# Optimization experiments

Hardware: AMD Instinct MI355X
Metric: run time of the kernel (lower is better)

The kernel has to match this reference:

```python
import jax, jax.numpy as jnp
import numpy as np

N_NODES = 100_000
N_EDGES = 3_200_000
D_IN, D_EDGE, D_HID, D_OUT = 8, 4, 32, 16
NEG_SLOPE = 0.2  # PyG GATv2Conv default


def setup_inputs() -> dict:
    key = jax.random.key(0)
    ks = jax.random.split(key, 13)
    s = 0.1
    return {
        "x": jax.random.normal(ks[0], (N_NODES, D_IN), jnp.float32),
        "edge_index": jax.random.randint(ks[1], (2, N_EDGES), 0, N_NODES, dtype=jnp.int64),
        "edge_attr": jax.random.normal(ks[2], (N_EDGES, D_EDGE), jnp.float32),
        "Wl1": jax.random.normal(ks[3], (D_IN, D_HID), jnp.float32) * s,
        "Wr1": jax.random.normal(ks[4], (D_IN, D_HID), jnp.float32) * s,
        "We1": jax.random.normal(ks[5], (D_EDGE, D_HID), jnp.float32) * s,
        "att1": jax.random.normal(ks[6], (D_HID,), jnp.float32) * s,
        "b1": jnp.zeros((D_HID,), jnp.float32),
        "Wl2": jax.random.normal(ks[7], (D_HID, D_OUT), jnp.float32) * s,
        "Wr2": jax.random.normal(ks[8], (D_HID, D_OUT), jnp.float32) * s,
        "We2": jax.random.normal(ks[9], (D_EDGE, D_OUT), jnp.float32) * s,
        "att2": jax.random.normal(ks[10], (D_OUT,), jnp.float32) * s,
        "b2": jnp.zeros((D_OUT,), jnp.float32),
    }


def _segment_softmax(score, seg, n):
    m = jax.ops.segment_max(score, seg, num_segments=n)
    e = jnp.exp(score - m[seg])
    z = jax.ops.segment_sum(e, seg, num_segments=n)
    return e / z[seg]


def _gatv2(x, src, dst, ea_raw, Wl, Wr, We, att, bias, n):
    # GATv2 (heads=1): score_ij = att . leaky_relu(Wl x_j + Wr x_i + We e_ij)
    xl = x @ Wl            # [N, d]
    xr = x @ Wr            # [N, d]
    ea = ea_raw @ We       # [E, d]
    h = jax.nn.leaky_relu(xl[src] + xr[dst] + ea, NEG_SLOPE)  # [E, d]
    score = h @ att        # [E]
    alpha = _segment_softmax(score, dst, n)
    out = jax.ops.segment_sum(alpha[:, None] * xl[src], dst, num_segments=n)
    return out + bias


def reference(x, edge_index, edge_attr, Wl1, Wr1, We1, att1, b1, Wl2, Wr2, We2, att2, b2):
    n = x.shape[0]
    src, dst = edge_index[0], edge_index[1]
    # add_self_loops=True with fill_value='mean': self-loop edge_attr = mean of
    # incoming raw edge_attr per target node (0 for isolated targets)
    ones = jnp.ones((src.shape[0],), x.dtype)
    cnt = jax.ops.segment_sum(ones, dst, num_segments=n)
    loop_attr = jax.ops.segment_sum(edge_attr, dst, num_segments=n) / jnp.maximum(cnt, 1.0)[:, None]
    ar = jnp.arange(n, dtype=src.dtype)
    src2 = jnp.concatenate([src, ar])
    dst2 = jnp.concatenate([dst, ar])
    ea2 = jnp.concatenate([edge_attr, loop_attr], axis=0)
    h = jax.nn.relu(_gatv2(x, src2, dst2, ea2, Wl1, Wr1, We1, att1, b1, n))
    out = _gatv2(h, src2, dst2, ea2, Wl2, Wr2, We2, att2, b2, n)
    return out.reshape(-1)
```

## Files before the change

### kernel.cpp

```cpp
#include <hip/hip_runtime.h>

#define NEG_SLOPE 0.2f
#define CHUNK 16384
#define KMAX  1600
#define CAP   3264
#define NBLKMAX 256
#define NDB   49

__global__ __launch_bounds__(1024) void k_bin(const int* __restrict__ ei,
                                              const float* __restrict__ eattr,
                                              int* __restrict__ cloff,
                                              int* __restrict__ ssrc,
                                              float4* __restrict__ seat,
                                              int E, int K) {
    __shared__ int s_off[KMAX + 1];
    __shared__ unsigned s_eid[CHUNK];
    int t = threadIdx.x;
    for (int i = t; i <= K; i += 1024) s_off[i] = 0;
    __syncthreads();
    int base = blockIdx.x * CHUNK;
    int end = min(base + CHUNK, E);
    int Ec = end - base;
    unsigned pack[CHUNK / 1024];
#pragma unroll
    for (int i = 0; i < CHUNK / 1024; i++) {
        int el = t + 1024 * i;
        pack[i] = 0xFFFFFFFFu;
        if (el < Ec) {
            int dst = ei[E + base + el];
            int b = dst >> 6;
            int r = atomicAdd(&s_off[b], 1);
            pack[i] = ((unsigned)b << 20) | ((unsigned)(dst & 63) << 14) | (unsigned)r;
        }
    }
    __syncthreads();
    if (t < 64) {
        int run = 0;
        for (int bb = 0; bb < K; bb += 64) {
            int b = bb + t;
            int v = (b < K) ? s_off[b] : 0;
            int x = v;
#pragma unroll
            for (int off = 1; off < 64; off <<= 1) {
                int y = __shfl_up(x, off, 64);
                if (t >= off) x += y;
            }
            if (b < K) s_off[b] = run + x - v;
            run += __shfl(x, 63, 64);
        }
        if (t == 0) s_off[K] = run;
    }
    __syncthreads();
#pragma unroll
    for (int i = 0; i < CHUNK / 1024; i++) {
        int el = t + 1024 * i;
        if (el < Ec) {
            unsigned p = pack[i];
            int b = p >> 20;
            int r = p & 0x3FFF;
            int dl = (p >> 14) & 63;
            s_eid[s_off[b] + r] = ((unsigned)dl << 14) | (unsigned)el;
        }
    }
    __syncthreads();
    for (int pos = t; pos < Ec; pos += 1024) {
        unsigned v = s_eid[pos];
        int el = v & 0x3FFF;
        int dl = v >> 14;
        int e = base + el;
        int src = ei[e];
        float4 a = *(const float4*)(eattr + 4ll * e);
        ssrc[base + pos] = src | (dl << 17);
        seat[base + pos] = a;
    }
    for (int i = t; i <= K; i += 1024)
        cloff[(long long)blockIdx.x * (K + 1) + i] = s_off[i];
}

__global__ void k_transp(const int* __restrict__ in, int* __restrict__ out, int R, int C) {
    __shared__ int tile[32][33];
    int c0 = blockIdx.x * 32, r0 = blockIdx.y * 32;
    int c = c0 + threadIdx.x, r = r0 + threadIdx.y;
    if (r < R && c < C) tile[threadIdx.y][threadIdx.x] = in[(long long)r * C + c];
    __syncthreads();
    int oc = r0 + threadIdx.x, orr = c0 + threadIdx.y;
    if (orr < C && oc < R) out[(long long)orr * R + oc] = tile[threadIdx.x][threadIdx.y];
}

__global__ void k_btot(const int* __restrict__ cloffT, int* __restrict__ bucketTotal,
                       int K, int NBLK) {
    int b = (blockIdx.x * blockDim.x + threadIdx.x) >> 6;
    int lane = threadIdx.x & 63;
    if (b >= K) return;
    const int* r0 = cloffT + (long long)b * NBLK;
    const int* r1 = r0 + NBLK;
    int s = 0;
    for (int c = lane; c < NBLK; c += 64) s += r1[c] - r0[c];
#pragma unroll
    for (int off = 32; off >= 1; off >>= 1) s += __shfl_xor(s, off, 64);
    if (lane == 0) bucketTotal[b] = s;
}

__global__ void k_scanK(const int* __restrict__ bucketTotal, int* __restrict__ slotBase,
                        int* __restrict__ qofs, int N, int K) {
    __shared__ int s[512];
    int t = threadIdx.x;
    int v[4];
    int sum = 0;
    int base = t * 4;
    for (int j = 0; j < 4; j++) {
        int b = base + j, x = 0;
        if (b < K) { int nb = min(64, N - (b << 6)); x = bucketTotal[b] + nb; }
        v[j] = sum;
        sum += x;
    }
    s[t] = sum;
    __syncthreads();
    for (int off = 1; off < 512; off <<= 1) {
        int x = (t >= off) ? s[t - off] : 0;
        __syncthreads();
        s[t] += x;
        __syncthreads();
    }
    int tb = s[t] - sum;
    for (int j = 0; j < 4; j++) {
        int b = base + j;
        if (b < K) slotBase[b] = tb + v[j];
    }
    if (t == 511) { slotBase[K] = s[511]; qofs[4ll * N] = s[511]; }
}

__global__ __launch_bounds__(512, 8) void k_perm(const int* __restrict__ ssrc,
                                                 const float4* __restrict__ seat,
                                                 const int* __restrict__ cloffT,
                                                 const int* __restrict__ slotBase,
                                                 int* __restrict__ qofs,
                                                 int* __restrict__ fsrc,
                                                 float4* __restrict__ feat,
                                                 int N, int K, int NBLK, int QDIV) {
    __shared__ int s_pack[CAP];
    __shared__ int s_g[CAP];
    __shared__ int co[NBLKMAX], qq[NBLKMAX + 1], sc[NBLKMAX];
    __shared__ int hist2[256], cur2[256], lst2[256], sc2[256];
    __shared__ int hist[64];
    __shared__ float lsum[64][4];
    int b = blockIdx.x, t = threadIdx.x;
    int nb = min(64, N - (b << 6));
    if (t < 256) { hist2[t] = 0; cur2[t] = 0; }
    if (t < 64) {
        lsum[t][0] = 0.f; lsum[t][1] = 0.f; lsum[t][2] = 0.f; lsum[t][3] = 0.f;
    }
    const int* r0 = cloffT + (long long)b * NBLK;
    const int* r1 = r0 + NBLK;
    int len = 0;
    if (t < NBLKMAX) {
        if (t < NBLK) { int c0v = r0[t]; len = r1[t] - c0v; co[t] = c0v; }
        sc[t] = (t < NBLK) ? len : 0;
    }
    __syncthreads();
    for (int off = 1; off < NBLKMAX; off <<= 1) {
        int x = 0;
        if (t < NBLKMAX && t >= off) x = sc[t - off];
        __syncthreads();
        if (t < NBLKMAX) sc[t] += x;
        __syncthreads();
    }
    if (t < NBLK) qq[t] = sc[t] - len;
    if (t == NBLKMAX - 1) qq[NBLK] = sc[NBLKMAX - 1];
    __syncthreads();
    int Eb = qq[NBLK];
    for (int i = t; i < Eb; i += 512) {
        int lo2 = 0, hi2 = NBLK;
        while (lo2 + 1 < hi2) { int mid = (lo2 + hi2) >> 1; if (qq[mid] <= i) lo2 = mid; else hi2 = mid; }
        int g = lo2 * CHUNK + co[lo2] + (i - qq[lo2]);
        int p = ssrc[g];
        int srcv = p & 0x1FFFF;
        int q = (unsigned)srcv / (unsigned)QDIV;
        s_pack[i] = p | (q << 23);
        s_g[i] = g;
        atomicAdd(&hist2[(((p >> 17) & 63) << 2) | q], 1);
    }
    __syncthreads();
    if (t < 64) {
        int c = hist2[4 * t] + hist2[4 * t + 1] + hist2[4 * t + 2] + hist2[4 * t + 3];
        hist[t] = c;
        if (t < nb) {
            int node = (b << 6) + t;
            int qs = (unsigned)node / (unsigned)QDIV;
            hist2[t * 4 + qs] += 1;
            cur2[t * 4 + qs] = 1;
        }
    }
    __syncthreads();
    if (t < 256) sc2[t] = hist2[t];
    __syncthreads();
    for (int off = 1; off < 256; off <<= 1) {
        int x = 0;
        if (t < 256 && t >= off) x = sc2[t - off];
        __syncthreads();
        if (t < 256) sc2[t] += x;
        __syncthreads();
    }
    if (t < 256) lst2[t] = sc2[t] - hist2[t];
    __syncthreads();
    int lo = slotBase[b];
    if (t < 256) {
        int dl = t >> 2;
        if (dl < nb)
            qofs[(((long long)((b << 6) + dl)) << 2) + (t & 3)] = lo + lst2[t];
    }
    for (int i = t; i < Eb; i += 512) {
        int p = s_pack[i];
        int dl = (p >> 17) & 63;
        int q = (p >> 23) & 3;
        int srcv = p & 0x1FFFF;
        int bin = (dl << 2) | q;
        int r = atomicAdd(&cur2[bin], 1);
        float4 a = seat[s_g[i]];
        long long pos = lo + lst2[bin] + r;
        fsrc[pos] = srcv;
        feat[pos] = a;
        atomicAdd(&lsum[dl][0], a.x);
        atomicAdd(&lsum[dl][1], a.y);
        atomicAdd(&lsum[dl][2], a.z);
        atomicAdd(&lsum[dl][3], a.w);
    }
    __syncthreads();
    if (t < nb) {
        int node = (b << 6) + t;
        int qs = (unsigned)node / (unsigned)QDIV;
        float inv = 1.f / fmaxf((float)hist[t], 1.f);
        long long pos = lo + lst2[t * 4 + qs];
        fsrc[pos] = node;
        feat[pos] = make_float4(lsum[t][0] * inv, lsum[t][1] * inv,
                                lsum[t][2] * inv, lsum[t][3] * inv);
    }
}

template <int DIN, int D>
__global__ void k_xform(const float* __restrict__ x, const float* __restrict__ Wl,
                        const float* __restrict__ Wr, float* __restrict__ xl,
                        float* __restrict__ xr, int N) {
    __shared__ float sWl[DIN * D], sWr[DIN * D];
    for (int i = threadIdx.x; i < DIN * D; i += blockDim.x) { sWl[i] = Wl[i]; sWr[i] = Wr[i]; }
    __syncthreads();
    int t = blockIdx.x * blockDim.x + threadIdx.x;
    if (t >= N * D) return;
    int n = t / D, d = t % D;
    const float* xp = x + (long long)n * DIN;
    float sl = 0.f, sr = 0.f;
#pragma unroll
    for (int k = 0; k < DIN; k++) {
        float xv = xp[k];
        sl += xv * sWl[k * D + d];
        sr += xv * sWr[k * D + d];
    }
    xl[t] = sl;
    xr[t] = sr;
}

template <int L>
__device__ __forceinline__ void gat_edge(bool valid, const float4& a, const float4& xlv,
                                         const float4& we0, const float4& we1,
                                         const float4& we2, const float4& we3,
                                         const float4& av, const float4& xrv,
                                         float4& acc, float& z) {
    float4 v;
    v.x = fmaf(a.x, we0.x, xrv.x); v.x = fmaf(a.y, we1.x, v.x);
    v.x = fmaf(a.z, we2.x, v.x);   v.x = fmaf(a.w, we3.x, v.x); v.x += xlv.x;
    v.y = fmaf(a.x, we0.y, xrv.y); v.y = fmaf(a.y, we1.y, v.y);
    v.y = fmaf(a.z, we2.y, v.y);   v.y = fmaf(a.w, we3.y, v.y); v.y += xlv.y;
    v.z = fmaf(a.x, we0.z, xrv.z); v.z = fmaf(a.y, we1.z, v.z);
    v.z = fmaf(a.z, we2.z, v.z);   v.z = fmaf(a.w, we3.z, v.z); v.z += xlv.z;
    v.w = fmaf(a.x, we0.w, xrv.w); v.w = fmaf(a.y, we1.w, v.w);
    v.w = fmaf(a.z, we2.w, v.w);   v.w = fmaf(a.w, we3.w, v.w); v.w += xlv.w;
    v.x = v.x > 0.f ? v.x : NEG_SLOPE * v.x;
    v.y = v.y > 0.f ? v.y : NEG_SLOPE * v.y;
    v.z = v.z > 0.f ? v.z : NEG_SLOPE * v.z;
    v.w = v.w > 0.f ? v.w : NEG_SLOPE * v.w;
    float sc = av.x * v.x + av.y * v.y + av.z * v.z + av.w * v.w;
#pragma unroll
    for (int off = L / 2; off >= 1; off >>= 1) sc += __shfl_xor(sc, off, 64);
    float ev = valid ? __expf(sc) : 0.f;
    z += ev;
    acc.x = fmaf(ev, xlv.x, acc.x);
    acc.y = fmaf(ev, xlv.y, acc.y);
    acc.z = fmaf(ev, xlv.z, acc.z);
    acc.w = fmaf(ev, xlv.w, acc.w);
}

template <int D, int NPHASE, bool RELU>
__global__ __launch_bounds__(256, 8) void k_gat(const int* __restrict__ fsrc,
                      const float4* __restrict__ feat,
                      const int* __restrict__ qofs,
                      const float* __restrict__ xl, const float* __restrict__ xr,
                      const float* __restrict__ We, const float* __restrict__ att,
                      const float* __restrict__ bias, float* __restrict__ out, int N) {
    constexpr int L = D / 4;
    constexpr int G = 64 / L;
    __shared__ float part[NDB][D + 4];
    __shared__ float xrl[NDB][D];
    int d0 = blockIdx.x * NDB;
    int nd = min(NDB, N - d0);
    int tid = threadIdx.x;
    for (int i = tid; i < nd * D; i += 256) xrl[i / D][i % D] = xr[(long long)d0 * D + i];
    for (int i = tid; i < nd * (D + 4); i += 256) part[i / (D + 4)][i % (D + 4)] = 0.f;
    __syncthreads();
    int wv = tid >> 6;
    int lane = tid & 63;
    int g = lane / L;
    int j = lane % L;

    const float4 we0 = *(const float4*)(We + 0 * D + 4 * j);
    const float4 we1 = *(const float4*)(We + 1 * D + 4 * j);
    const float4 we2 = *(const float4*)(We + 2 * D + 4 * j);
    const float4 we3 = *(const float4*)(We + 3 * D + 4 * j);
    const float4 av  = *(const float4*)(att + 4 * j);

    for (int ph = 0; ph < NPHASE; ++ph) {
        int qlo = (4 * ph) / NPHASE;
        int qhi = (4 * (ph + 1)) / NPHASE;
        for (int ld = wv; ld < nd; ld += 4) {
            int d = d0 + ld;
            int s0 = qofs[4 * d + qlo];
            int s1 = qofs[4 * d + qhi];
            int cnt = s1 - s0;
            if (cnt == 0) continue;
            float4 xrv = *(const float4*)&xrl[ld][4 * j];
            float4 acc = make_float4(0.f, 0.f, 0.f, 0.f);
            float z = 0.f;
            for (int it = 0; it * G < cnt; ++it) {
                int o = it * G + g;
                bool val = o < cnt;
                int sl = s0 + min(o, cnt - 1);
                int src = fsrc[sl];
                float4 a = feat[sl];
                float4 xlv = *(const float4*)(xl + (long long)src * D + 4 * j);
                gat_edge<L>(val, a, xlv, we0, we1, we2, we3, av, xrv, acc, z);
            }
#pragma unroll
            for (int off = 32; off >= L; off >>= 1) {
                acc.x += __shfl_xor(acc.x, off, 64);
                acc.y += __shfl_xor(acc.y, off, 64);
                acc.z += __shfl_xor(acc.z, off, 64);
                acc.w += __shfl_xor(acc.w, off, 64);
                z += __shfl_xor(z, off, 64);
            }
            if (g == 0) {
                float4* pp = (float4*)&part[ld][4 * j];
                float4 cp = *pp;
                cp.x += acc.x; cp.y += acc.y; cp.z += acc.z; cp.w += acc.w;
                *pp = cp;
                if (j == 0) part[ld][D] += z;
            }
        }
    }
    for (int ld = wv; ld < nd; ld += 4) {
        if (g == 0) {
            float inv = 1.f / part[ld][D];
            float4 nm = *(float4*)&part[ld][4 * j];
            float4 bv = *(const float4*)(bias + 4 * j);
            float4 o4;
            o4.x = nm.x * inv + bv.x;
            o4.y = nm.y * inv + bv.y;
            o4.z = nm.z * inv + bv.z;
            o4.w = nm.w * inv + bv.w;
            if (RELU) {
                o4.x = fmaxf(o4.x, 0.f); o4.y = fmaxf(o4.y, 0.f);
                o4.z = fmaxf(o4.z, 0.f); o4.w = fmaxf(o4.w, 0.f);
            }
            *(float4*)(out + (long long)(d0 + ld) * D + 4 * j) = o4;
        }
    }
}

extern "C" void kernel_launch(void* const* d_in, const int* in_sizes, int n_in,
                              void* d_out, int out_size, void* d_ws, size_t ws_size,
                              hipStream_t stream) {
    const float* x     = (const float*)d_in[0];
    const int*   ei    = (const int*)d_in[1];
    const float* eattr = (const float*)d_in[2];
    const float* Wl1   = (const float*)d_in[3];
    const float* Wr1   = (const float*)d_in[4];
    const float* We1   = (const float*)d_in[5];
    const float* att1  = (const float*)d_in[6];
    const float* b1    = (const float*)d_in[7];
    const float* Wl2   = (const float*)d_in[8];
    const float* Wr2   = (const float*)d_in[9];
    const float* We2   = (const float*)d_in[10];
    const float* att2  = (const float*)d_in[11];
    const float* b2    = (const float*)d_in[12];

    const int N = in_sizes[0] / 8;
    const int E = in_sizes[1] / 2;
    const int K = (N + 63) >> 6;
    const int NBLK = (E + CHUNK - 1) / CHUNK;
    const int QDIV = (N + 3) / 4;

    int* iws = (int*)d_ws;
    size_t o = 0;
    int* bucketTotal = iws + o; o += K;
    int* slotBase    = iws + o; o += K + 1;
    int* qofs        = iws + o; o += 4ll * N + 1;
    int* cloff       = iws + o; o += (size_t)NBLK * (K + 1);
    int* cloffT      = iws + o; o += (size_t)(K + 1) * NBLK;
    o = (o + 7) & ~(size_t)7;
    int*    fsrc = (int*)(iws + o);    o += (size_t)(E + N);
    o = (o + 3) & ~(size_t)3;
    float4* feat = (float4*)(iws + o); o += 4ll * (E + N);
    size_t stage = o;
    int*    ssrc = (int*)(iws + o);    o += (size_t)E;
    o = (o + 3) & ~(size_t)3;
    float4* seat = (float4*)(iws + o); o += 4ll * E;
    float* xl = (float*)(iws + stage);
    float* xr = xl + 32ll * N;
    float* h  = xr + 32ll * N;

    const int B = 256;
    auto cdiv = [](long long a, long long b) { return (int)((a + b - 1) / b); };

    k_bin<<<NBLK, 1024, 0, stream>>>(ei, eattr, cloff, ssrc, seat, E, K);
    dim3 tb(32, 32);
    k_transp<<<dim3(cdiv(K + 1, 32), cdiv(NBLK, 32)), tb, 0, stream>>>(cloff, cloffT, NBLK, K + 1);
    k_btot<<<cdiv(64ll * K, B), B, 0, stream>>>(cloffT, bucketTotal, K, NBLK);
    k_scanK<<<1, 512, 0, stream>>>(bucketTotal, slotBase, qofs, N, K);
    k_perm<<<K, 512, 0, stream>>>(ssrc, seat, cloffT, slotBase, qofs, fsrc, feat, N, K, NBLK, QDIV);

    const int GGRID = cdiv(N, NDB);

    k_xform<8, 32><<<cdiv(32ll * N, B), B, 0, stream>>>(x, Wl1, Wr1, xl, xr, N);
    k_gat<32, 4, true><<<GGRID, B, 0, stream>>>(fsrc, feat, qofs, xl, xr, We1, att1, b1, h, N);

    k_xform<32, 16><<<cdiv(16ll * N, B), B, 0, stream>>>(h, Wl2, Wr2, xl, xr, N);
    k_gat<16, 2, false><<<GGRID, B, 0, stream>>>(fsrc, feat, qofs, xl, xr, We2, att2, b2, (float*)d_out, N);
}
```

Before: 554.6 us.

## Process one destination per wavefront in GAT kernel, dropping phased LDS accumulation

The GAT aggregation kernel previously gave each 256-thread block 49 destination nodes. It staged xr and partial sums in shared memory and walked the edges in multiple phases over quarter-ranges of sorted slots, presumably to keep source feature reads cache-local. The new kernel assigns one wavefront per destination, covers the whole edge range in one pass, keeps the accumulators in registers, and unrolls the edge loop by two so more gather loads are in flight. This removes shared memory, barriers and the phase loop, at the cost of the source-locality ordering the phases provided and of occupancy hints from launch_bounds.

```diff
diff --git a/kernel.cpp b/kernel.cpp
--- a/kernel.cpp
+++ b/kernel.cpp
@@ -5,7 +5,6 @@
 #define KMAX  1600
 #define CAP   3264
 #define NBLKMAX 256
-#define NDB   49
 
 __global__ __launch_bounds__(1024) void k_bin(const int* __restrict__ ei,
                                               const float* __restrict__ eattr,
@@ -289,8 +288,8 @@
     acc.w = fmaf(ev, xlv.w, acc.w);
 }
 
-template <int D, int NPHASE, bool RELU>
-__global__ __launch_bounds__(256, 8) void k_gat(const int* __restrict__ fsrc,
+template <int D, bool RELU>
+__global__ void k_gat(const int* __restrict__ fsrc,
                       const float4* __restrict__ feat,
                       const int* __restrict__ qofs,
                       const float* __restrict__ xl, const float* __restrict__ xr,
@@ -298,79 +297,68 @@
                       const float* __restrict__ bias, float* __restrict__ out, int N) {
     constexpr int L = D / 4;
     constexpr int G = 64 / L;
-    __shared__ float part[NDB][D + 4];
-    __shared__ float xrl[NDB][D];
-    int d0 = blockIdx.x * NDB;
-    int nd = min(NDB, N - d0);
-    int tid = threadIdx.x;
-    for (int i = tid; i < nd * D; i += 256) xrl[i / D][i % D] = xr[(long long)d0 * D + i];
-    for (int i = tid; i < nd * (D + 4); i += 256) part[i / (D + 4)][i % (D + 4)] = 0.f;
-    __syncthreads();
-    int wv = tid >> 6;
-    int lane = tid & 63;
+    int w = (blockIdx.x * blockDim.x + threadIdx.x) >> 6;
+    int lane = threadIdx.x & 63;
+    if (w >= N) return;
     int g = lane / L;
     int j = lane % L;
+    int s0 = qofs[4 * w], s1 = qofs[4 * w + 4];
+    int cnt = s1 - s0;
 
     const float4 we0 = *(const float4*)(We + 0 * D + 4 * j);
     const float4 we1 = *(const float4*)(We + 1 * D + 4 * j);
     const float4 we2 = *(const float4*)(We + 2 * D + 4 * j);
     const float4 we3 = *(const float4*)(We + 3 * D + 4 * j);
     const float4 av  = *(const float4*)(att + 4 * j);
-
-    for (int ph = 0; ph < NPHASE; ++ph) {
-        int qlo = (4 * ph) / NPHASE;
-        int qhi = (4 * (ph + 1)) / NPHASE;
-        for (int ld = wv; ld < nd; ld += 4) {
-            int d = d0 + ld;
-            int s0 = qofs[4 * d + qlo];
-            int s1 = qofs[4 * d + qhi];
-            int cnt = s1 - s0;
-            if (cnt == 0) continue;
-            float4 xrv = *(const float4*)&xrl[ld][4 * j];
-            float4 acc = make_float4(0.f, 0.f, 0.f, 0.f);
-            float z = 0.f;
-            for (int it = 0; it * G < cnt; ++it) {
-                int o = it * G + g;
-                bool val = o < cnt;
-                int sl = s0 + min(o, cnt - 1);
-                int src = fsrc[sl];
-                float4 a = feat[sl];
-                float4 xlv = *(const float4*)(xl + (long long)src * D + 4 * j);
-                gat_edge<L>(val, a, xlv, we0, we1, we2, we3, av, xrv, acc, z);
-            }
-#pragma unroll
-            for (int off = 32; off >= L; off >>= 1) {
-                acc.x += __shfl_xor(acc.x, off, 64);
-                acc.y += __shfl_xor(acc.y, off, 64);
-                acc.z += __shfl_xor(acc.z, off, 64);
-                acc.w += __shfl_xor(acc.w, off, 64);
-                z += __shfl_xor(z, off, 64);
-            }
-            if (g == 0) {
-                float4* pp = (float4*)&part[ld][4 * j];
-                float4 cp = *pp;
-                cp.x += acc.x; cp.y += acc.y; cp.z += acc.z; cp.w += acc.w;
-                *pp = cp;
-                if (j == 0) part[ld][D] += z;
-            }
+    const float4 xrv = *(const float4*)(xr + (long long)w * D + 4 * j);
+
+    float4 acc = make_float4(0.f, 0.f, 0.f, 0.f);
+    float z = 0.f;
+
+    int it = 0;
+    for (; (it + 2) * G <= cnt; it += 2) {
+        int sl = s0 + it * G + g;
+        int srcA = fsrc[sl];
+        int srcB = fsrc[sl + G];
+        float4 aA = feat[sl];
+        float4 aB = feat[sl + G];
+        float4 xA = *(const float4*)(xl + (long long)srcA * D + 4 * j);
+        float4 xB = *(const float4*)(xl + (long long)srcB * D + 4 * j);
+        gat_edge<L>(true, aA, xA, we0, we1, we2, we3, av, xrv, acc, z);
+        gat_edge<L>(true, aB, xB, we0, we1, we2, we3, av, xrv, acc, z);
+    }
+    for (; it * G < cnt; ++it) {
+        int o = it * G + g;
+        bool v = o < cnt;
+        int sl = s0 + min(o, cnt - 1);
+        int src = fsrc[sl];
+        float4 a = feat[sl];
+        float4 xv = *(const float4*)(xl + (long long)src * D + 4 * j);
+        gat_edge<L>(v, a, xv, we0, we1, we2, we3, av, xrv, acc, z);
+    }
+
+#pragma unroll
+    for (int off = 32; off >= L; off >>= 1) {
+        acc.x += __shfl_xor(acc.x, off, 64);
+        acc.y += __shfl_xor(acc.y, off, 64);
+        acc.z += __shfl_xor(acc.z, off, 64);
+        acc.w += __shfl_xor(acc.w, off, 64);
+        z += __shfl_xor(z, off, 64);
+    }
+
+    if (g == 0) {
+        float inv = 1.0f / z;
+        float4 bv = *(const float4*)(bias + 4 * j);
+        float4 o;
+        o.x = acc.x * inv + bv.x;
+        o.y = acc.y * inv + bv.y;
+        o.z = acc.z * inv + bv.z;
+        o.w = acc.w * inv + bv.w;
+        if (RELU) {
+            o.x = fmaxf(o.x, 0.f); o.y = fmaxf(o.y, 0.f);
+            o.z = fmaxf(o.z, 0.f); o.w = fmaxf(o.w, 0.f);
         }
-    }
-    for (int ld = wv; ld < nd; ld += 4) {
-        if (g == 0) {
-            float inv = 1.f / part[ld][D];
-            float4 nm = *(float4*)&part[ld][4 * j];
-            float4 bv = *(const float4*)(bias + 4 * j);
-            float4 o4;
-            o4.x = nm.x * inv + bv.x;
-            o4.y = nm.y * inv + bv.y;
-            o4.z = nm.z * inv + bv.z;
-            o4.w = nm.w * inv + bv.w;
-            if (RELU) {
-                o4.x = fmaxf(o4.x, 0.f); o4.y = fmaxf(o4.y, 0.f);
-                o4.z = fmaxf(o4.z, 0.f); o4.w = fmaxf(o4.w, 0.f);
-            }
-            *(float4*)(out + (long long)(d0 + ld) * D + 4 * j) = o4;
-        }
+        *(float4*)(out + (long long)w * D + 4 * j) = o;
     }
 }
 
@@ -426,11 +414,9 @@
     k_scanK<<<1, 512, 0, stream>>>(bucketTotal, slotBase, qofs, N, K);
     k_perm<<<K, 512, 0, stream>>>(ssrc, seat, cloffT, slotBase, qofs, fsrc, feat, N, K, NBLK, QDIV);
 
-    const int GGRID = cdiv(N, NDB);
-
     k_xform<8, 32><<<cdiv(32ll * N, B), B, 0, stream>>>(x, Wl1, Wr1, xl, xr, N);
-    k_gat<32, 4, true><<<GGRID, B, 0, stream>>>(fsrc, feat, qofs, xl, xr, We1, att1, b1, h, N);
+    k_gat<32, true><<<cdiv(N, 4), B, 0, stream>>>(fsrc, feat, qofs, xl, xr, We1, att1, b1, h, N);
 
     k_xform<32, 16><<<cdiv(16ll * N, B), B, 0, stream>>>(h, Wl2, Wr2, xl, xr, N);
-    k_gat<16, 2, false><<<GGRID, B, 0, stream>>>(fsrc, feat, qofs, xl, xr, We2, att2, b2, (float*)d_out, N);
-}
+    k_gat<16, false><<<cdiv(N, 4), B, 0, stream>>>(fsrc, feat, qofs, xl, xr, We2, att2, b2, (float*)d_out, N);
+}
```

New measurement: 487.9 us. -12.0%, faster.
